# Optimization experiments

Hardware: AMD Instinct MI355X
Metric: run time of the kernel (lower is better)

The kernel has to match this reference:

```python
import jax, jax.numpy as jnp
import numpy as np

EPS = 1e-12  # matches torch.nn.functional.normalize default eps

def _l2_normalize(x):
    # F.normalize: x / max(||x||_2, eps)
    n = jnp.sqrt(jnp.sum(x * x, axis=-1, keepdims=True))
    return x / jnp.maximum(n, EPS)

def setup_inputs() -> dict:
    key = jax.random.key(0)
    k1, k2, k3, k4, k5 = jax.random.split(key, 5)
    B, N, D, V = 2048, 50000, 256, 256
    return {
        "query": jax.random.normal(k1, (B, D), dtype=jnp.float32),
        "W": jax.random.normal(k2, (D, D), dtype=jnp.float32) * (1.0 / np.sqrt(D)),
        "b": jax.random.normal(k3, (D,), dtype=jnp.float32) * 0.01,
        "keys": jax.random.normal(k4, (N, D), dtype=jnp.float32),
        "values": jax.random.normal(k5, (N, V), dtype=jnp.float32),
        "usage": jnp.ones((N,), dtype=jnp.float32),
        "top_k": 8,
    }

def reference(query, W, b, keys, values, usage, top_k):
    # q = Linear(query)  (store is full: n_stored == capacity, so no padding branch)
    q = query @ W.T + b                      # (B, D)
    q_norm = _l2_normalize(q)                # (B, D)
    k_norm = _l2_normalize(keys)             # (N, D)
    sim = q_norm @ k_norm.T                  # (B, N) cosine similarity
    scores, indices = jax.lax.top_k(sim, top_k)   # (B, K), (B, K)
    retrieved_values = values[indices]       # (B, K, V) gather
    # usage counter update: +1 per retrieved index (duplicates accumulate)
    usage_new = usage.at[indices.reshape(-1)].add(1.0)
    return retrieved_values, scores, usage_new
```

## Files before the change

### kernel.cpp

```cpp
#include <hip/hip_runtime.h>

#define D 256
#define NKEYS 50000
#define KCHUNK 256
#define NCHUNK 196
#define NKPAD (KCHUNK * NCHUNK)
#define BQ 2048
#define NC (NCHUNK * 4)
#define NCAND 16
#define DNEG_INF (-1.0e300)

typedef __attribute__((ext_vector_type(8))) __bf16 bf16x8;
typedef __attribute__((ext_vector_type(16))) float f32x16;

__device__ __forceinline__ unsigned short f2bf(float x) {
  unsigned int u = __float_as_uint(x);
  unsigned int r = (u + 0x7fffu + ((u >> 16) & 1u)) >> 16;
  return (unsigned short)r;
}

__device__ __forceinline__ unsigned int med3u(unsigned int a, unsigned int b, unsigned int c) {
  unsigned int d;
  asm("v_med3_u32 %0, %1, %2, %3" : "=v"(d) : "v"(a), "v"(b), "v"(c));
  return d;
}

__global__ __launch_bounds__(256) void prep_kernel(const float* __restrict__ query,
                                                   const float* __restrict__ W,
                                                   const float* __restrict__ b,
                                                   const float* __restrict__ keys,
                                                   const float* __restrict__ usage,
                                                   unsigned short* __restrict__ qbf,
                                                   double* __restrict__ q64n,
                                                   double* __restrict__ kinv64,
                                                   unsigned short* __restrict__ kbf,
                                                   float* __restrict__ out_u) {
  __shared__ __align__(16) float As[8][20];
  __shared__ __align__(16) float Bs[256][20];
  if (blockIdx.x < 256) {
    const int tid = threadIdx.x;
    const int qt = tid >> 5;
    const int nt = tid & 31;
    const int m0 = blockIdx.x * 8;

    double acc[8];
#pragma unroll
    for (int j = 0; j < 8; j++) acc[j] = 0.0;

    for (int k0 = 0; k0 < D; k0 += 16) {
      if (tid < 32) {
        int r = tid >> 2, f = tid & 3;
        *(float4*)(&As[r][f * 4]) = *(const float4*)(&query[(m0 + r) * D + k0 + f * 4]);
      }
#pragma unroll
      for (int i = 0; i < 4; i++) {
        int r = (tid >> 2) + 64 * i, f = tid & 3;
        *(float4*)(&Bs[r][f * 4]) = *(const float4*)(&W[r * D + k0 + f * 4]);
      }
      __syncthreads();
#pragma unroll
      for (int kk = 0; kk < 16; kk += 4) {
        float4 af = *(const float4*)(&As[qt][kk]);
#pragma unroll
        for (int j = 0; j < 8; j++) {
          float4 bf = *(const float4*)(&Bs[nt + 32 * j][kk]);
          acc[j] = fma((double)af.x, (double)bf.x, acc[j]);
          acc[j] = fma((double)af.y, (double)bf.y, acc[j]);
          acc[j] = fma((double)af.z, (double)bf.z, acc[j]);
          acc[j] = fma((double)af.w, (double)bf.w, acc[j]);
        }
      }
      __syncthreads();
    }
#pragma unroll
    for (int j = 0; j < 8; j++) acc[j] += (double)b[nt + 32 * j];

    double s = 0.0;
#pragma unroll
    for (int j = 0; j < 8; j++) s = fma(acc[j], acc[j], s);
#pragma unroll
    for (int m = 16; m; m >>= 1) s += __shfl_xor(s, m, 32);
    double den = fmax(sqrt(s), 1e-12);
    int row = m0 + qt;
#pragma unroll
    for (int j = 0; j < 8; j++) {
      double v = acc[j] / den;
      q64n[row * D + nt + 32 * j] = v;
      qbf[row * D + nt + 32 * j] = f2bf((float)v);
    }
  } else {
    int wave = threadIdx.x >> 6, lane = threadIdx.x & 63;
    int r = (blockIdx.x - 256) * 4 + wave;
    if (r >= NKPAD) return;
    if (lane == 0 && r < NKEYS) out_u[r] = usage[r];
    int e = lane * 4;
    int e2 = e ^ ((r & 31) << 3);
    unsigned short* dst = kbf + (long long)r * D + e2;
    if (r >= NKEYS) {
      ushort4 z = {0, 0, 0, 0};
      *(ushort4*)dst = z;
      return;
    }
    float4 v = *(const float4*)(&keys[(long long)r * D + e]);
    double s = (double)v.x * v.x + (double)v.y * v.y + (double)v.z * v.z + (double)v.w * v.w;
#pragma unroll
    for (int m = 32; m; m >>= 1) s += __shfl_xor(s, m, 64);
    double inv = 1.0 / fmax(sqrt(s), 1e-12);
    if (lane == 0) kinv64[r] = inv;
    float fi = (float)inv;
    ushort4 o;
    o.x = f2bf(v.x * fi); o.y = f2bf(v.y * fi); o.z = f2bf(v.z * fi); o.w = f2bf(v.w * fi);
    *(ushort4*)dst = o;
  }
}

__global__ __launch_bounds__(256, 4) void sim_mfma_kernel(const unsigned short* __restrict__ qbf,
                                                          const unsigned short* __restrict__ kbf,
                                                          unsigned int* __restrict__ cand_p) {
  __shared__ __align__(16) unsigned char klds[2][16384];
  const int bid = blockIdx.x;
  const int k8 = bid & 7;
  const int ii = bid >> 3;
  const int qt = ii & 15;
  const int chunk = (ii >> 4) * 8 + k8;
  if (chunk >= NCHUNK) return;
  const int n0 = chunk * KCHUNK;
  const int m0 = qt * 128;

  const int tid = threadIdx.x;
  const int w = tid >> 6;
  const int l = tid & 63;
  const int col = l & 31;
  const int hi = l >> 5;
  const int qrow = m0 + w * 32 + col;

  bf16x8 qf[16];
#pragma unroll
  for (int ks = 0; ks < 16; ks++)
    qf[ks] = *(const bf16x8*)(qbf + (long long)qrow * D + ks * 16 + hi * 8);

  unsigned int s0 = 0u, s1 = 0u, s2 = 0u, s3 = 0u;
  const bool edge = (n0 + KCHUNK > NKEYS);
  const int rbase = col * 512 + hi * 16;
  const int swz = col << 4;
  const char* kchunk = (const char*)kbf + (long long)n0 * 512;

  auto prefetch = [&](unsigned char* buf, int kst) {
#pragma unroll
    for (int i = 0; i < 4; i++) {
      int dstbase = i * 4096 + w * 1024;
      int off = dstbase + l * 16;
      const void* src = kchunk + (long long)(kst * 32 + (off >> 9)) * 512 + (off & 511);
      __builtin_amdgcn_global_load_lds(src, (void*)(buf + dstbase), 16, 0, 0);
    }
  };

  auto compute = [&](const unsigned char* buf, int st) {
    f32x16 acc;
#pragma unroll
    for (int r = 0; r < 16; r++) acc[r] = 2.0f;
#pragma unroll
    for (int ks = 0; ks < 16; ks++) {
      bf16x8 a = *(const bf16x8*)(buf + ((rbase + ks * 32) ^ swz));
      acc = __builtin_amdgcn_mfma_f32_32x32x16_bf16(a, qf[ks], acc, 0, 0, 0);
    }
#pragma unroll
    for (int r = 0; r < 16; r++) {
      unsigned int u = __float_as_uint(acc[r]);
      int slot = st * 32 + (r & 3) + 8 * (r >> 2) + 4 * hi;
      unsigned int v = (u & 0xFFFFFF00u) | (unsigned)slot;
      if (edge && (n0 + slot >= NKEYS)) v = 0u;
      unsigned int n1 = med3u(s0, s1, v);
      unsigned int n2 = med3u(s1, s2, v);
      unsigned int n3 = med3u(s2, s3, v);
      s0 = max(s0, v);
      s1 = n1; s2 = n2; s3 = n3;
    }
  };

  prefetch(&klds[0][0], 0);

#pragma unroll 1
  for (int st = 0; st < 7; st++) {
    prefetch(&klds[(st + 1) & 1][0], st + 1);
    asm volatile("s_waitcnt vmcnt(4)" ::: "memory");
    __builtin_amdgcn_s_barrier();
    __builtin_amdgcn_sched_barrier(0);
    compute(&klds[st & 1][0], st);
    __builtin_amdgcn_sched_barrier(0);
    __builtin_amdgcn_s_barrier();
  }
  asm volatile("s_waitcnt vmcnt(0)" ::: "memory");
  __builtin_amdgcn_s_barrier();
  __builtin_amdgcn_sched_barrier(0);
  compute(&klds[1][0], 7);

  unsigned int b0 = (unsigned int)__shfl_xor((int)s0, 32, 64);
  unsigned int b1 = (unsigned int)__shfl_xor((int)s1, 32, 64);
  unsigned int b2 = (unsigned int)__shfl_xor((int)s2, 32, 64);
  unsigned int b3 = (unsigned int)__shfl_xor((int)s3, 32, 64);
  unsigned int t0 = max(s0, b3), t1 = max(s1, b2), t2 = max(s2, b1), t3 = max(s3, b0);
  unsigned int u0 = max(t0, t2), u2 = min(t0, t2), u1 = max(t1, t3), u3 = min(t1, t3);
  unsigned int w0 = max(u0, u1), w1 = min(u0, u1), w2 = max(u2, u3), w3 = min(u2, u3);

  if (hi == 0) {
    uint4 o = {w0, w1, w2, w3};
    long long base = (long long)qrow * NC + chunk * 4;
    *(uint4*)(cand_p + base) = o;
  }
}

__global__ __launch_bounds__(256) void finalize_kernel(const unsigned int* __restrict__ cand_p,
                                                       const double* __restrict__ q64n,
                                                       const float* __restrict__ keys,
                                                       const double* __restrict__ kinv64,
                                                       const float* __restrict__ values,
                                                       float* __restrict__ scores_out,
                                                       float* __restrict__ out_rv,
                                                       float* __restrict__ usage_out) {
  __shared__ int f8s[4][8];
  const int wv = threadIdx.x >> 6;
  const int l = threadIdx.x & 63;
  const int q = blockIdx.x * 4 + wv;

  unsigned int lv[13];
  int li[13];
#pragma unroll
  for (int s = 0; s < 13; s++) {
    int c = l + 64 * s;
    if (c < NC) {
      unsigned int p = cand_p[(long long)q * NC + c];
      lv[s] = p;
      li[s] = (c >> 2) * KCHUNK + (int)(p & 255u);
    } else { lv[s] = 0u; li[s] = 0x7fffffff; }
  }
  int myidx = 0;
#pragma unroll 1
  for (int r = 0; r < NCAND; r++) {
    unsigned int bv = 0u;
    int bi = 0x7fffffff;
#pragma unroll
    for (int s = 0; s < 13; s++)
      if (lv[s] > bv || (lv[s] == bv && li[s] < bi)) { bv = lv[s]; bi = li[s]; }
#pragma unroll
    for (int m = 32; m; m >>= 1) {
      unsigned int ov = (unsigned int)__shfl_xor((int)bv, m, 64);
      int oi = __shfl_xor(bi, m, 64);
      if (ov > bv || (ov == bv && oi < bi)) { bv = ov; bi = oi; }
    }
    if (l == r) myidx = bi;
#pragma unroll
    for (int s = 0; s < 13; s++)
      if (li[s] == bi) lv[s] = 0u;
  }

  const int sub = l & 7;
  const double* qr = &q64n[(long long)q * D + sub * 32];
  double qv[32];
#pragma unroll
  for (int t = 0; t < 32; t++) qv[t] = qr[t];
  double scp[2];
#pragma unroll 1
  for (int p = 0; p < 2; p++) {
    int cand = p * 8 + (l >> 3);
    int idx = __shfl(myidx, cand, 64);
    const float* kr = &keys[(long long)idx * D + sub * 32];
    double s = 0.0;
#pragma unroll
    for (int t = 0; t < 32; t++) s = fma(qv[t], (double)kr[t], s);
#pragma unroll
    for (int m = 4; m; m >>= 1) s += __shfl_xor(s, m, 8);
    scp[p] = s * kinv64[idx];
  }

  double a0 = __shfl(scp[0], (l & 7) * 8, 64);
  double a1 = __shfl(scp[1], (l & 7) * 8, 64);
  double myv = (l < 8) ? a0 : a1;
  int rank = 0;
#pragma unroll
  for (int t = 0; t < NCAND; t++) {
    double tv = __shfl(myv, t, 64);
    int ti = __shfl(myidx, t, 64);
    if (tv > myv || (tv == myv && ti < myidx)) rank++;
  }
  if (l < NCAND && rank < 8) {
    scores_out[q * 8 + rank] = (float)myv;
    atomicAdd(&usage_out[myidx], 1.0f);
    f8s[wv][rank] = myidx;
  }
  __syncthreads();

  {
    const int row = l >> 3;
    const int c0 = sub * 32;
    int idx = f8s[wv][row];
    const float* vr = &values[(long long)idx * D + c0];
    float* orow = &out_rv[((long long)q * 8 + row) * D + c0];
#pragma unroll
    for (int t = 0; t < 8; t++)
      *(float4*)(&orow[t * 4]) = *(const float4*)(&vr[t * 4]);
  }
}

extern "C" void kernel_launch(void* const* d_in, const int* in_sizes, int n_in,
                              void* d_out, int out_size, void* d_ws, size_t ws_size,
                              hipStream_t stream) {
  (void)in_sizes; (void)n_in; (void)out_size; (void)ws_size;
  const float* query  = (const float*)d_in[0];
  const float* W      = (const float*)d_in[1];
  const float* b      = (const float*)d_in[2];
  const float* keys   = (const float*)d_in[3];
  const float* values = (const float*)d_in[4];
  const float* usage  = (const float*)d_in[5];

  float* out    = (float*)d_out;
  float* out_rv = out;
  float* out_sc = out + BQ * 8 * D;
  float* out_us = out_sc + BQ * 8;

  double*         q64n   = (double*)d_ws;
  double*         kinv64 = q64n + BQ * D;
  unsigned short* qbf    = (unsigned short*)(kinv64 + NKEYS);
  unsigned short* kbf    = qbf + BQ * D;
  unsigned int*   cand_p = (unsigned int*)(kbf + (long long)NKPAD * D);

  hipLaunchKernelGGL(prep_kernel, dim3(256 + NKPAD / 4), dim3(256), 0, stream,
                     query, W, b, keys, usage, qbf, q64n, kinv64, kbf, out_us);
  hipLaunchKernelGGL(sim_mfma_kernel, dim3(3200), dim3(256), 0, stream, qbf, kbf, cand_p);
  hipLaunchKernelGGL(finalize_kernel, dim3(BQ / 4), dim3(256), 0, stream, cand_p, q64n, keys, kinv64, values, out_sc, out_rv, out_us);
}
```

Measured before the change: 131.6 us.

## Double query rows per wave to reuse each key LDS fragment across two MFMAs

Each wave now handles 64 query rows instead of 32, so each block covers 256 queries and the grid halves to 1600 blocks. Every key fragment read from LDS feeds two MFMAs, one per query sub-tile, with separate top-4 candidate registers for each. The aim is to halve key-tile global loads and LDS reads per query and to raise MFMA density. The cost is doubled query-fragment and accumulator register use, with launch bounds lowered to 2 blocks per CU, which reduces occupancy and latency hiding.

```diff
diff --git a/kernel.cpp b/kernel.cpp
--- a/kernel.cpp
+++ b/kernel.cpp
@@ -114,32 +114,36 @@
   }
 }
 
-__global__ __launch_bounds__(256, 4) void sim_mfma_kernel(const unsigned short* __restrict__ qbf,
+__global__ __launch_bounds__(256, 2) void sim_mfma_kernel(const unsigned short* __restrict__ qbf,
                                                           const unsigned short* __restrict__ kbf,
                                                           unsigned int* __restrict__ cand_p) {
   __shared__ __align__(16) unsigned char klds[2][16384];
   const int bid = blockIdx.x;
   const int k8 = bid & 7;
   const int ii = bid >> 3;
-  const int qt = ii & 15;
-  const int chunk = (ii >> 4) * 8 + k8;
+  const int qt = ii & 7;
+  const int chunk = (ii >> 3) * 8 + k8;
   if (chunk >= NCHUNK) return;
   const int n0 = chunk * KCHUNK;
-  const int m0 = qt * 128;
+  const int m0 = qt * 256;
 
   const int tid = threadIdx.x;
   const int w = tid >> 6;
   const int l = tid & 63;
   const int col = l & 31;
   const int hi = l >> 5;
-  const int qrow = m0 + w * 32 + col;
-
-  bf16x8 qf[16];
-#pragma unroll
-  for (int ks = 0; ks < 16; ks++)
-    qf[ks] = *(const bf16x8*)(qbf + (long long)qrow * D + ks * 16 + hi * 8);
-
-  unsigned int s0 = 0u, s1 = 0u, s2 = 0u, s3 = 0u;
+  const int qrow0 = m0 + w * 64 + col;
+  const int qrow1 = qrow0 + 32;
+
+  bf16x8 qfA[16], qfB[16];
+#pragma unroll
+  for (int ks = 0; ks < 16; ks++) {
+    qfA[ks] = *(const bf16x8*)(qbf + (long long)qrow0 * D + ks * 16 + hi * 8);
+    qfB[ks] = *(const bf16x8*)(qbf + (long long)qrow1 * D + ks * 16 + hi * 8);
+  }
+
+  unsigned int sa0 = 0u, sa1 = 0u, sa2 = 0u, sa3 = 0u;
+  unsigned int sb0 = 0u, sb1 = 0u, sb2 = 0u, sb3 = 0u;
   const bool edge = (n0 + KCHUNK > NKEYS);
   const int rbase = col * 512 + hi * 16;
   const int swz = col << 4;
@@ -156,25 +160,31 @@
   };
 
   auto compute = [&](const unsigned char* buf, int st) {
-    f32x16 acc;
-#pragma unroll
-    for (int r = 0; r < 16; r++) acc[r] = 2.0f;
+    f32x16 acc0, acc1;
+#pragma unroll
+    for (int r = 0; r < 16; r++) { acc0[r] = 2.0f; acc1[r] = 2.0f; }
 #pragma unroll
     for (int ks = 0; ks < 16; ks++) {
       bf16x8 a = *(const bf16x8*)(buf + ((rbase + ks * 32) ^ swz));
-      acc = __builtin_amdgcn_mfma_f32_32x32x16_bf16(a, qf[ks], acc, 0, 0, 0);
+      acc0 = __builtin_amdgcn_mfma_f32_32x32x16_bf16(a, qfA[ks], acc0, 0, 0, 0);
+      acc1 = __builtin_amdgcn_mfma_f32_32x32x16_bf16(a, qfB[ks], acc1, 0, 0, 0);
     }
 #pragma unroll
     for (int r = 0; r < 16; r++) {
-      unsigned int u = __float_as_uint(acc[r]);
       int slot = st * 32 + (r & 3) + 8 * (r >> 2) + 4 * hi;
-      unsigned int v = (u & 0xFFFFFF00u) | (unsigned)slot;
-      if (edge && (n0 + slot >= NKEYS)) v = 0u;
-      unsigned int n1 = med3u(s0, s1, v);
-      unsigned int n2 = med3u(s1, s2, v);
-      unsigned int n3 = med3u(s2, s3, v);
-      s0 = max(s0, v);
-      s1 = n1; s2 = n2; s3 = n3;
+      bool kill = edge && (n0 + slot >= NKEYS);
+      unsigned int vA = (__float_as_uint(acc0[r]) & 0xFFFFFF00u) | (unsigned)slot;
+      if (kill) vA = 0u;
+      unsigned int a1 = med3u(sa0, sa1, vA);
+      unsigned int a2 = med3u(sa1, sa2, vA);
+      unsigned int a3 = med3u(sa2, sa3, vA);
+      sa0 = max(sa0, vA); sa1 = a1; sa2 = a2; sa3 = a3;
+      unsigned int vB = (__float_as_uint(acc1[r]) & 0xFFFFFF00u) | (unsigned)slot;
+      if (kill) vB = 0u;
+      unsigned int b1 = med3u(sb0, sb1, vB);
+      unsigned int b2 = med3u(sb1, sb2, vB);
+      unsigned int b3 = med3u(sb2, sb3, vB);
+      sb0 = max(sb0, vB); sb1 = b1; sb2 = b2; sb3 = b3;
     }
   };
 
@@ -195,18 +205,30 @@
   __builtin_amdgcn_sched_barrier(0);
   compute(&klds[1][0], 7);
 
-  unsigned int b0 = (unsigned int)__shfl_xor((int)s0, 32, 64);
-  unsigned int b1 = (unsigned int)__shfl_xor((int)s1, 32, 64);
-  unsigned int b2 = (unsigned int)__shfl_xor((int)s2, 32, 64);
-  unsigned int b3 = (unsigned int)__shfl_xor((int)s3, 32, 64);
-  unsigned int t0 = max(s0, b3), t1 = max(s1, b2), t2 = max(s2, b1), t3 = max(s3, b0);
-  unsigned int u0 = max(t0, t2), u2 = min(t0, t2), u1 = max(t1, t3), u3 = min(t1, t3);
-  unsigned int w0 = max(u0, u1), w1 = min(u0, u1), w2 = max(u2, u3), w3 = min(u2, u3);
+  {
+    unsigned int b0 = (unsigned int)__shfl_xor((int)sa0, 32, 64);
+    unsigned int b1 = (unsigned int)__shfl_xor((int)sa1, 32, 64);
+    unsigned int b2 = (unsigned int)__shfl_xor((int)sa2, 32, 64);
+    unsigned int b3 = (unsigned int)__shfl_xor((int)sa3, 32, 64);
+    unsigned int t0 = max(sa0, b3), t1 = max(sa1, b2), t2 = max(sa2, b1), t3 = max(sa3, b0);
+    unsigned int u0 = max(t0, t2), u2 = min(t0, t2), u1 = max(t1, t3), u3 = min(t1, t3);
+    sa0 = max(u0, u1); sa1 = min(u0, u1); sa2 = max(u2, u3); sa3 = min(u2, u3);
+  }
+  {
+    unsigned int b0 = (unsigned int)__shfl_xor((int)sb0, 32, 64);
+    unsigned int b1 = (unsigned int)__shfl_xor((int)sb1, 32, 64);
+    unsigned int b2 = (unsigned int)__shfl_xor((int)sb2, 32, 64);
+    unsigned int b3 = (unsigned int)__shfl_xor((int)sb3, 32, 64);
+    unsigned int t0 = max(sb0, b3), t1 = max(sb1, b2), t2 = max(sb2, b1), t3 = max(sb3, b0);
+    unsigned int u0 = max(t0, t2), u2 = min(t0, t2), u1 = max(t1, t3), u3 = min(t1, t3);
+    sb0 = max(u0, u1); sb1 = min(u0, u1); sb2 = max(u2, u3); sb3 = min(u2, u3);
+  }
 
   if (hi == 0) {
-    uint4 o = {w0, w1, w2, w3};
-    long long base = (long long)qrow * NC + chunk * 4;
-    *(uint4*)(cand_p + base) = o;
+    uint4 oA = {sa0, sa1, sa2, sa3};
+    uint4 oB = {sb0, sb1, sb2, sb3};
+    *(uint4*)(cand_p + (long long)qrow0 * NC + chunk * 4) = oA;
+    *(uint4*)(cand_p + (long long)qrow1 * NC + chunk * 4) = oB;
   }
 }
 
@@ -326,6 +348,6 @@
 
   hipLaunchKernelGGL(prep_kernel, dim3(256 + NKPAD / 4), dim3(256), 0, stream,
                      query, W, b, keys, usage, qbf, q64n, kinv64, kbf, out_us);
-  hipLaunchKernelGGL(sim_mfma_kernel, dim3(3200), dim3(256), 0, stream, qbf, kbf, cand_p);
+  hipLaunchKernelGGL(sim_mfma_kernel, dim3(1600), dim3(256), 0, stream, qbf, kbf, cand_p);
   hipLaunchKernelGGL(finalize_kernel, dim3(BQ / 4), dim3(256), 0, stream, cand_p, q64n, keys, kinv64, values, out_sc, out_rv, out_us);
 }
```

Result: no change. 134.0 us (+1.8%).
